# Performance work log

Hardware: AMD Instinct MI355X
Metric: run time of the kernel (lower is better)

## Reference

```python
import jax, jax.numpy as jnp
import numpy as np


def setup_inputs() -> dict:
    key = jax.random.key(0)
    k_w, k_e = jax.random.split(key)
    NUM_EDGE_TYPES = 8
    NUM_CHANNELS = 4
    NUM_NODES = 4096
    NUM_EDGES = 262144  # per edge type, avg degree 64
    weights = jax.random.normal(k_w, (NUM_CHANNELS, NUM_EDGE_TYPES), dtype=jnp.float32)
    edge_index = jax.random.randint(k_e, (NUM_EDGE_TYPES, 2, NUM_EDGES), 0, NUM_NODES, dtype=jnp.int64)
    return {"weights": weights, "edge_index": edge_index, "num_nodes": NUM_NODES}


def reference(weights, edge_index, num_nodes):
    # to_dense_adj: scatter-add ones into an [N, N] dense adjacency per edge type
    def dense_adj(ei):  # ei: [2, num_edges]
        A = jnp.zeros((num_nodes, num_nodes), dtype=jnp.float32)
        return A.at[ei[0], ei[1]].add(1.0)

    A_stack = jax.vmap(dense_adj)(edge_index)          # [E, N, N]
    soft_weights = jax.nn.softmax(weights, axis=-1)    # [C, E]
    A_meta = jnp.einsum('ce,enm->cnm', soft_weights, A_stack)  # [C, N, N]
    return A_meta, soft_weights
```

## Files before the change

### kernel.cpp

```cpp
#include <hip/hip_runtime.h>

#define N_NODES   4096
#define NUM_ET    8
#define NUM_CH    4
#define NUM_EDGES 262144
#define NN        ((size_t)N_NODES * N_NODES)
#define A_SIZE    (NUM_CH * NN)

#define P1_BLOCKS   256
#define P1_THREADS  1024
#define EDGES_PER_BLOCK (NUM_ET * NUM_EDGES / P1_BLOCKS)
#define CHUNKS_PER_TYPE (NUM_EDGES / EDGES_PER_BLOCK)
#define NGROUPS     2048
#define SLOT_CAP    24
#define SLOT_STRIDE 32

typedef float vfloat4 __attribute__((ext_vector_type(4)));

__global__ __launch_bounds__(P1_THREADS) void bin_edges(
        const int* __restrict__ ei,
        unsigned short* __restrict__ slots) {
    __shared__ unsigned int lcnt[NGROUPS];
    const int t   = threadIdx.x;
    const int blk = blockIdx.x;

    for (int g = t; g < NGROUPS; g += P1_THREADS) lcnt[g] = 0;
    __syncthreads();

    const int e     = blk / CHUNKS_PER_TYPE;
    const int chunk = blk % CHUNKS_PER_TYPE;
    const int* srcb = ei + (size_t)(2 * e) * NUM_EDGES + chunk * EDGES_PER_BLOCK;
    const int* dstb = srcb + NUM_EDGES;
    const unsigned int tag = (unsigned int)e << 12;

    #pragma unroll
    for (int j = 0; j < EDGES_PER_BLOCK / (4 * P1_THREADS); ++j) {
        int off = j * (4 * P1_THREADS) + t * 4;
        int4 s4 = *(const int4*)(srcb + off);
        int4 d4 = *(const int4*)(dstb + off);
        int ss[4] = {s4.x, s4.y, s4.z, s4.w};
        int dd[4] = {d4.x, d4.y, d4.z, d4.w};
        #pragma unroll
        for (int k = 0; k < 4; ++k) {
            int g = ss[k] >> 1;
            unsigned pos = atomicAdd(&lcnt[g], 1u);
            if (pos < SLOT_CAP) {
                slots[((size_t)g * P1_BLOCKS + blk) * SLOT_STRIDE + pos] =
                    (unsigned short)(((unsigned)(ss[k] & 1) << 15) | tag | (unsigned)dd[k]);
            }
        }
    }
    __syncthreads();
    for (int g = t; g < NGROUPS; g += P1_THREADS)
        slots[((size_t)g * P1_BLOCKS + blk) * SLOT_STRIDE + 31] =
            (unsigned short)min(lcnt[g], (unsigned)SLOT_CAP);
}

__global__ __launch_bounds__(256) void expand_groups(
        const float* __restrict__ w,
        const unsigned short* __restrict__ slots,
        float* __restrict__ out) {
    __shared__ unsigned int cnt[2 * N_NODES];
    __shared__ float swl_s[NUM_CH * NUM_ET];
    const int t = threadIdx.x;
    const int g = blockIdx.x;

    const uint4* rs = (const uint4*)(slots + (size_t)g * P1_BLOCKS * SLOT_STRIDE);
    uint4 q0 = rs[t * 4 + 0];
    uint4 q1 = rs[t * 4 + 1];
    uint4 q2 = rs[t * 4 + 2];
    uint4 q3 = rs[t * 4 + 3];

    for (int i = t; i < 2 * N_NODES; i += 256) cnt[i] = 0;
    if (t < NUM_CH) {
        float v[NUM_ET];
        float m = -1e30f;
        #pragma unroll
        for (int e = 0; e < NUM_ET; ++e) {
            v[e] = w[t * NUM_ET + e];
            m = fmaxf(m, v[e]);
        }
        float s = 0.0f;
        #pragma unroll
        for (int e = 0; e < NUM_ET; ++e) { v[e] = expf(v[e] - m); s += v[e]; }
        float inv = 1.0f / s;
        #pragma unroll
        for (int e = 0; e < NUM_ET; ++e) swl_s[t * NUM_ET + e] = v[e] * inv;
    }
    __syncthreads();

    int n = (int)(q3.w >> 16);
    unsigned su[12] = {q0.x, q0.y, q0.z, q0.w,
                       q1.x, q1.y, q1.z, q1.w,
                       q2.x, q2.y, q2.z, q2.w};
    #pragma unroll
    for (int wd = 0; wd < 12; ++wd) {
        int b2 = 2 * wd;
        if (b2 < n) {
            unsigned v = su[wd] & 0xFFFFu;
            atomicAdd(&cnt[((v >> 15) << 12) + (v & 4095u)],
                      1u << (4 * ((v >> 12) & 7u)));
            if (b2 + 1 < n) {
                v = su[wd] >> 16;
                atomicAdd(&cnt[((v >> 15) << 12) + (v & 4095u)],
                          1u << (4 * ((v >> 12) & 7u)));
            }
        }
    }
    __syncthreads();

    float swl[NUM_CH][NUM_ET];
    #pragma unroll
    for (int c = 0; c < NUM_CH; ++c)
        #pragma unroll
        for (int e = 0; e < NUM_ET; ++e)
            swl[c][e] = swl_s[c * NUM_ET + e];

    #pragma unroll
    for (int r1 = 0; r1 < 2; ++r1) {
        const size_t rowbase = (size_t)(2 * g + r1) * N_NODES;
        #pragma unroll
        for (int j = 0; j < 4; ++j) {
            int cell = j * 1024 + t * 4;
            uint4 wq = *(const uint4*)&cnt[r1 * N_NODES + cell];
            unsigned wk[4] = {wq.x, wq.y, wq.z, wq.w};
            float o[NUM_CH][4];
            #pragma unroll
            for (int k = 0; k < 4; ++k) {
                float a0 = 0.f, a1 = 0.f, a2 = 0.f, a3 = 0.f;
                #pragma unroll
                for (int e = 0; e < NUM_ET; ++e) {
                    float f = (float)((wk[k] >> (4 * e)) & 0xFu);
                    a0 += swl[0][e] * f;
                    a1 += swl[1][e] * f;
                    a2 += swl[2][e] * f;
                    a3 += swl[3][e] * f;
                }
                o[0][k] = a0; o[1][k] = a1; o[2][k] = a2; o[3][k] = a3;
            }
            #pragma unroll
            for (int c = 0; c < NUM_CH; ++c) {
                vfloat4 v4 = {o[c][0], o[c][1], o[c][2], o[c][3]};
                __builtin_nontemporal_store(
                    v4, (vfloat4*)(out + (size_t)c * NN + rowbase + cell));
            }
        }
    }

    if (g == 0 && t < NUM_CH * NUM_ET) out[A_SIZE + t] = swl_s[t];
}

extern "C" void kernel_launch(void* const* d_in, const int* in_sizes, int n_in,
                              void* d_out, int out_size, void* d_ws, size_t ws_size,
                              hipStream_t stream) {
    const float* weights = (const float*)d_in[0];
    const int*   ei      = (const int*)d_in[1];
    float* out = (float*)d_out;

    unsigned short* slots = (unsigned short*)d_ws;

    bin_edges<<<P1_BLOCKS, P1_THREADS, 0, stream>>>(ei, slots);
    expand_groups<<<NGROUPS, 256, 0, stream>>>(weights, slots, out);
}
```

Measured before the change: 322.2 us.

## Stage bins in LDS, coalesce slot writes, add overflow list, expand four rows per block

Binning now collects each group's records in shared memory and writes them as two 16-byte stores per group in a block-major layout, replacing scattered 2-byte global stores. Slot capacity drops to 15, and extra edges go to a global overflow list through a global atomic counter. The expand kernel now handles four rows per block (1024 blocks), reading slots for two groups per thread and scanning the whole overflow list. The risks are the extra memset launch, global atomic contention on overflow, every block re-scanning the overflow list, and a 64KB shared counter array that lowers occupancy.

```diff
diff --git a/kernel.cpp b/kernel.cpp
--- a/kernel.cpp
+++ b/kernel.cpp
@@ -7,20 +7,24 @@
 #define NN        ((size_t)N_NODES * N_NODES)
 #define A_SIZE    (NUM_CH * NN)
 
+#define NGROUPS     2048
 #define P1_BLOCKS   256
 #define P1_THREADS  1024
 #define EDGES_PER_BLOCK (NUM_ET * NUM_EDGES / P1_BLOCKS)
 #define CHUNKS_PER_TYPE (NUM_EDGES / EDGES_PER_BLOCK)
-#define NGROUPS     2048
-#define SLOT_CAP    24
-#define SLOT_STRIDE 32
+#define SLOT_CAP    15
+#define REG_U16     16
+#define OVF_CAP     16384
 
 typedef float vfloat4 __attribute__((ext_vector_type(4)));
 
 __global__ __launch_bounds__(P1_THREADS) void bin_edges(
         const int* __restrict__ ei,
-        unsigned short* __restrict__ slots) {
-    __shared__ unsigned int lcnt[NGROUPS];
+        unsigned short* __restrict__ slots,
+        unsigned int* __restrict__ ovf_cnt,
+        unsigned int* __restrict__ ovf) {
+    __shared__ unsigned short sslot[NGROUPS * REG_U16];
+    __shared__ unsigned int   lcnt[NGROUPS];
     const int t   = threadIdx.x;
     const int blk = blockIdx.x;
 
@@ -31,7 +35,7 @@
     const int chunk = blk % CHUNKS_PER_TYPE;
     const int* srcb = ei + (size_t)(2 * e) * NUM_EDGES + chunk * EDGES_PER_BLOCK;
     const int* dstb = srcb + NUM_EDGES;
-    const unsigned int tag = (unsigned int)e << 12;
+    const unsigned tag = (unsigned)e << 12;
 
     #pragma unroll
     for (int j = 0; j < EDGES_PER_BLOCK / (4 * P1_THREADS); ++j) {
@@ -43,35 +47,47 @@
         #pragma unroll
         for (int k = 0; k < 4; ++k) {
             int g = ss[k] >> 1;
+            unsigned rec = ((unsigned)(ss[k] & 1) << 15) | tag | (unsigned)dd[k];
             unsigned pos = atomicAdd(&lcnt[g], 1u);
             if (pos < SLOT_CAP) {
-                slots[((size_t)g * P1_BLOCKS + blk) * SLOT_STRIDE + pos] =
-                    (unsigned short)(((unsigned)(ss[k] & 1) << 15) | tag | (unsigned)dd[k]);
+                sslot[g * REG_U16 + pos] = (unsigned short)rec;
+            } else {
+                unsigned ix = atomicAdd(ovf_cnt, 1u);
+                if (ix < OVF_CAP) ovf[ix] = ((unsigned)g << 16) | rec;
             }
         }
     }
     __syncthreads();
-    for (int g = t; g < NGROUPS; g += P1_THREADS)
-        slots[((size_t)g * P1_BLOCKS + blk) * SLOT_STRIDE + 31] =
-            (unsigned short)min(lcnt[g], (unsigned)SLOT_CAP);
+
+    for (int g = t; g < NGROUPS; g += P1_THREADS) {
+        uint4 a = *(const uint4*)&sslot[g * REG_U16];
+        uint4 b = *(const uint4*)&sslot[g * REG_U16 + 8];
+        unsigned c = min(lcnt[g], (unsigned)SLOT_CAP);
+        b.w = (b.w & 0xFFFFu) | (c << 16);
+        uint4* dp = (uint4*)(slots + ((size_t)blk * NGROUPS + g) * REG_U16);
+        dp[0] = a;
+        dp[1] = b;
+    }
 }
 
-__global__ __launch_bounds__(256) void expand_groups(
+__global__ __launch_bounds__(256) void expand_quads(
         const float* __restrict__ w,
         const unsigned short* __restrict__ slots,
+        const unsigned int* __restrict__ ovf_cnt,
+        const unsigned int* __restrict__ ovf,
         float* __restrict__ out) {
-    __shared__ unsigned int cnt[2 * N_NODES];
+    __shared__ unsigned int cnt[4 * N_NODES];
     __shared__ float swl_s[NUM_CH * NUM_ET];
     const int t = threadIdx.x;
-    const int g = blockIdx.x;
+    const int G = blockIdx.x;
 
-    const uint4* rs = (const uint4*)(slots + (size_t)g * P1_BLOCKS * SLOT_STRIDE);
-    uint4 q0 = rs[t * 4 + 0];
-    uint4 q1 = rs[t * 4 + 1];
-    uint4 q2 = rs[t * 4 + 2];
-    uint4 q3 = rs[t * 4 + 3];
+    const uint4* rp = (const uint4*)(slots + ((size_t)t * NGROUPS + 2 * G) * REG_U16);
+    uint4 q0 = rp[0];
+    uint4 q1 = rp[1];
+    uint4 q2 = rp[2];
+    uint4 q3 = rp[3];
 
-    for (int i = t; i < 2 * N_NODES; i += 256) cnt[i] = 0;
+    for (int i = t; i < 4 * N_NODES; i += 256) cnt[i] = 0;
     if (t < NUM_CH) {
         float v[NUM_ET];
         float m = -1e30f;
@@ -89,22 +105,36 @@
     }
     __syncthreads();
 
-    int n = (int)(q3.w >> 16);
-    unsigned su[12] = {q0.x, q0.y, q0.z, q0.w,
-                       q1.x, q1.y, q1.z, q1.w,
-                       q2.x, q2.y, q2.z, q2.w};
     #pragma unroll
-    for (int wd = 0; wd < 12; ++wd) {
-        int b2 = 2 * wd;
-        if (b2 < n) {
-            unsigned v = su[wd] & 0xFFFFu;
-            atomicAdd(&cnt[((v >> 15) << 12) + (v & 4095u)],
+    for (int h = 0; h < 2; ++h) {
+        uint4 qa = h ? q2 : q0;
+        uint4 qb = h ? q3 : q1;
+        int n = (int)(qb.w >> 16);
+        unsigned su[8] = {qa.x, qa.y, qa.z, qa.w, qb.x, qb.y, qb.z, qb.w};
+        #pragma unroll
+        for (int wd = 0; wd < 8; ++wd) {
+            int b2 = 2 * wd;
+            if (b2 < n) {
+                unsigned v = su[wd] & 0xFFFFu;
+                atomicAdd(&cnt[((2 * h + (int)(v >> 15)) << 12) + (v & 4095u)],
+                          1u << (4 * ((v >> 12) & 7u)));
+                if (b2 + 1 < n) {
+                    v = su[wd] >> 16;
+                    atomicAdd(&cnt[((2 * h + (int)(v >> 15)) << 12) + (v & 4095u)],
+                              1u << (4 * ((v >> 12) & 7u)));
+                }
+            }
+        }
+    }
+    unsigned novf = min(*ovf_cnt, (unsigned)OVF_CAP);
+    for (unsigned i = t; i < novf; i += 256) {
+        unsigned r32 = ovf[i];
+        unsigned g = r32 >> 16;
+        if ((int)(g >> 1) == G) {
+            unsigned v = r32 & 0xFFFFu;
+            int row_local = (int)((g & 1u) << 1) + (int)(v >> 15);
+            atomicAdd(&cnt[(row_local << 12) + (v & 4095u)],
                       1u << (4 * ((v >> 12) & 7u)));
-            if (b2 + 1 < n) {
-                v = su[wd] >> 16;
-                atomicAdd(&cnt[((v >> 15) << 12) + (v & 4095u)],
-                          1u << (4 * ((v >> 12) & 7u)));
-            }
         }
     }
     __syncthreads();
@@ -117,12 +147,12 @@
             swl[c][e] = swl_s[c * NUM_ET + e];
 
     #pragma unroll
-    for (int r1 = 0; r1 < 2; ++r1) {
-        const size_t rowbase = (size_t)(2 * g + r1) * N_NODES;
+    for (int r1 = 0; r1 < 4; ++r1) {
+        const size_t rowbase = (size_t)(4 * G + r1) * N_NODES;
         #pragma unroll
         for (int j = 0; j < 4; ++j) {
             int cell = j * 1024 + t * 4;
-            uint4 wq = *(const uint4*)&cnt[r1 * N_NODES + cell];
+            uint4 wq = *(const uint4*)&cnt[(r1 << 12) + cell];
             unsigned wk[4] = {wq.x, wq.y, wq.z, wq.w};
             float o[NUM_CH][4];
             #pragma unroll
@@ -147,7 +177,7 @@
         }
     }
 
-    if (g == 0 && t < NUM_CH * NUM_ET) out[A_SIZE + t] = swl_s[t];
+    if (G == 0 && t < NUM_CH * NUM_ET) out[A_SIZE + t] = swl_s[t];
 }
 
 extern "C" void kernel_launch(void* const* d_in, const int* in_sizes, int n_in,
@@ -157,8 +187,13 @@
     const int*   ei      = (const int*)d_in[1];
     float* out = (float*)d_out;
 
-    unsigned short* slots = (unsigned short*)d_ws;
+    char* ws = (char*)d_ws;
+    unsigned short* slots   = (unsigned short*)ws;
+    size_t slots_bytes      = (size_t)P1_BLOCKS * NGROUPS * REG_U16 * sizeof(unsigned short);
+    unsigned int*   ovf_cnt = (unsigned int*)(ws + slots_bytes);
+    unsigned int*   ovf     = ovf_cnt + 64;
 
-    bin_edges<<<P1_BLOCKS, P1_THREADS, 0, stream>>>(ei, slots);
-    expand_groups<<<NGROUPS, 256, 0, stream>>>(weights, slots, out);
+    hipMemsetAsync(ovf_cnt, 0, sizeof(unsigned int), stream);
+    bin_edges<<<P1_BLOCKS, P1_THREADS, 0, stream>>>(ei, slots, ovf_cnt, ovf);
+    expand_quads<<<N_NODES / 4, 256, 0, stream>>>(weights, slots, ovf_cnt, ovf, out);
 }
```

New measurement: 298.1 us. 7.5% less time.
